# Performance work log

Measured on AMD Instinct MI355X. Metric: run time of the kernel, lower is better.

## Reference

```python
import jax, jax.numpy as jnp
import numpy as np

B, N, K, D, H = 4, 8192, 16, 128, 4
DK = D // H  # key_dim = num_hiddens // num_heads
NEG_INF = -1e9


def setup_inputs() -> dict:
    key = jax.random.key(0)
    ks = jax.random.split(key, 16)
    s = 1.0 / np.sqrt(D)
    return {
        "vertex_feat": jax.random.normal(ks[0], (B, N, D), dtype=jnp.float32),
        "neighbors_idx": jax.random.randint(ks[1], (B, N, K), 0, N, dtype=jnp.int32),
        "valid_lens": jax.random.randint(ks[2], (B, N), 0, K, dtype=jnp.int32),
        # MultiHeadAttention projections (keras EinsumDense with bias)
        "Wq": (jax.random.normal(ks[3], (D, H, DK)) * s).astype(jnp.float32),
        "bq": jnp.zeros((H, DK), jnp.float32),
        "Wk": (jax.random.normal(ks[4], (D, H, DK)) * s).astype(jnp.float32),
        "bk": jnp.zeros((H, DK), jnp.float32),
        "Wv": (jax.random.normal(ks[5], (D, H, DK)) * s).astype(jnp.float32),
        "bv": jnp.zeros((H, DK), jnp.float32),
        "Wo": (jax.random.normal(ks[6], (H, DK, D)) * s).astype(jnp.float32),
        "bo": jnp.zeros((D,), jnp.float32),
        # MLP: Dense(D, relu) -> Dense(D)
        "W1": (jax.random.normal(ks[7], (D, D)) * s).astype(jnp.float32),
        "b1": jnp.zeros((D,), jnp.float32),
        "W2": (jax.random.normal(ks[8], (D, D)) * s).astype(jnp.float32),
        "b2": jnp.zeros((D,), jnp.float32),
    }


def reference(vertex_feat, neighbors_idx, valid_lens,
              Wq, bq, Wk, bk, Wv, bv, Wo, bo, W1, b1, W2, b2):
    # query: [B, N, 1, D]; gathered neighbors (batch_dims=1): [B, N, K, D]
    q = vertex_feat[:, :, None, :]
    neigh = jax.vmap(lambda vf, idx: vf[idx])(vertex_feat, neighbors_idx)
    value = jnp.concatenate([q, neigh], axis=2)  # [B, N, K+1, D]

    # per-head projections
    qh = jnp.einsum('bnqd,dhk->bnqhk', q, Wq) + bq      # [B,N,1,H,DK]
    kh = jnp.einsum('bnsd,dhk->bnshk', value, Wk) + bk  # [B,N,K+1,H,DK]
    vh = jnp.einsum('bnsd,dhk->bnshk', value, Wv) + bv

    # attention over the neighbor axis (attention_axes=(2,))
    scores = jnp.einsum('bnqhk,bnshk->bnhqs', qh, kh) / np.sqrt(DK)  # [B,N,H,1,K+1]
    # mask: positions < valid_lens + 1 (self + valid neighbors)
    pos = jnp.arange(K + 1)[None, None, :]                # [1,1,K+1]
    mask = pos < (valid_lens + 1)[:, :, None]             # [B,N,K+1] bool
    scores = scores + jnp.where(mask, 0.0, NEG_INF)[:, :, None, None, :]
    attn = jax.nn.softmax(scores, axis=-1)                # [B,N,H,1,K+1]

    ctx = jnp.einsum('bnhqs,bnshk->bnqhk', attn, vh)      # [B,N,1,H,DK]
    out = jnp.einsum('bnqhk,hkd->bnqd', ctx, Wo) + bo     # [B,N,1,D]
    out = out[:, :, 0, :]                                  # squeeze -> [B,N,D]

    # MLP (dropout inactive at inference)
    h = jax.nn.relu(out @ W1 + b1)
    new_vertex_feat = h @ W2 + b2
    return new_vertex_feat
```

## Files before the change

kernel.cpp:

```cpp
#include <hip/hip_runtime.h>
#include <math.h>

#define BB 4
#define NN 8192
#define KNB 16
#define DD 128
#define SS 17
#define M_TOT (BB*NN)
#define WPAD 136
#define KVS 256

typedef __attribute__((ext_vector_type(8))) short          bf8;
typedef __attribute__((ext_vector_type(4))) float          f4;
typedef __attribute__((ext_vector_type(4))) unsigned short u16x4;

static __device__ __forceinline__ unsigned short f2bf(float f) {
    unsigned u = __builtin_bit_cast(unsigned, f);
    u += 0x7fffu + ((u >> 16) & 1u);
    return (unsigned short)(u >> 16);
}
static __device__ __forceinline__ float bf2f_s(short h) {
    return __builtin_bit_cast(float, (unsigned)(unsigned short)h << 16);
}

__global__ __launch_bounds__(256) void cvt_wT(
    const float* __restrict__ Wq, const float* __restrict__ Wk,
    const float* __restrict__ Wv, const float* __restrict__ Wo,
    const float* __restrict__ W1, const float* __restrict__ W2,
    unsigned short* __restrict__ out)
{
    int m = blockIdx.x >> 4;
    const float* src = (m == 0) ? Wq : (m == 1) ? Wk : (m == 2) ? Wv
                     : (m == 3) ? Wo : (m == 4) ? W1 : W2;
    unsigned short* dst = out + m * 16384;
    int o = (blockIdx.x & 15) * 1024 + threadIdx.x * 4;
    int n = o >> 7, k = o & 127;
    u16x4 r;
    #pragma unroll
    for (int i = 0; i < 4; ++i) r[i] = f2bf(src[(size_t)(k + i) * 128 + n]);
    *(u16x4*)(dst + o) = r;
}

__global__ __launch_bounds__(256) void qkv_kernel(
    const float* __restrict__ X, const unsigned short* __restrict__ WtT,
    const float* __restrict__ bq, const float* __restrict__ bk,
    const float* __restrict__ bv,
    unsigned short* __restrict__ qh, unsigned short* __restrict__ kv)
{
    __shared__ unsigned short Xs[64 * WPAD];
    __shared__ unsigned short Wb[128 * WPAD];

    const int tid  = threadIdx.x;
    const int row0 = blockIdx.x * 64;

    {
        const f4* Xg = (const f4*)(X + (size_t)row0 * DD);
        #pragma unroll
        for (int i = 0; i < 8; ++i) {
            int idx = tid + i * 256;
            int r = idx >> 5, c4 = idx & 31;
            f4 v = __builtin_nontemporal_load(Xg + idx);
            u16x4 u;
            u[0] = f2bf(v.x); u[1] = f2bf(v.y); u[2] = f2bf(v.z); u[3] = f2bf(v.w);
            *(u16x4*)(Xs + r * WPAD + c4 * 4) = u;
        }
    }
    #pragma unroll
    for (int i = 0; i < 8; ++i) {
        int c = tid + i * 256;
        int n = c >> 4, k8 = c & 15;
        *(bf8*)(Wb + n * WPAD + k8 * 8) = ((const bf8*)WtT)[c];
    }

    const int lane = tid & 63, wv = tid >> 6;
    const int ln = lane & 15, quad = lane >> 4;
    __syncthreads();

    bf8 afr[4];
    #pragma unroll
    for (int s = 0; s < 4; ++s)
        afr[s] = *(const bf8*)(Xs + (wv * 16 + ln) * WPAD + s * 32 + quad * 8);

    #pragma unroll 1
    for (int g = 0; g < 3; ++g) {
        if (g > 0) {
            __syncthreads();
            const bf8* Wn = (const bf8*)(WtT + g * 16384);
            #pragma unroll
            for (int i = 0; i < 8; ++i) {
                int c = tid + i * 256;
                int n = c >> 4, k8 = c & 15;
                *(bf8*)(Wb + n * WPAD + k8 * 8) = Wn[c];
            }
            __syncthreads();
        }

        f4 acc[8] = {};
        #pragma unroll
        for (int t = 0; t < 8; ++t) {
            bf8 bfr[4];
            #pragma unroll
            for (int s = 0; s < 4; ++s)
                bfr[s] = *(const bf8*)(Wb + (t * 16 + ln) * WPAD + s * 32 + quad * 8);
            #pragma unroll
            for (int s = 0; s < 4; ++s)
                acc[t] = __builtin_amdgcn_mfma_f32_16x16x32_bf16(afr[s], bfr[s], acc[t], 0, 0, 0);
        }

        const float* bias = (g == 0) ? bq : (g == 1) ? bk : bv;
        unsigned short* Y;
        int ystride;
        if (g == 0) { Y = qh;       ystride = DD;  }
        else        { Y = kv + (g == 2 ? 128 : 0); ystride = KVS; }

        #pragma unroll
        for (int t = 0; t < 8; ++t) {
            int col = t * 16 + ln;
            float bc = bias[col];
            #pragma unroll
            for (int r = 0; r < 4; ++r) {
                int row = row0 + wv * 16 + quad * 4 + r;
                Y[(size_t)row * ystride + col] = f2bf(acc[t][r] + bc);
            }
        }
    }
}

__global__ __launch_bounds__(256) void attn_kernel(
    const unsigned short* __restrict__ Qh, const unsigned short* __restrict__ KV,
    const int* __restrict__ nbr, const int* __restrict__ vlen,
    unsigned short* __restrict__ Ctx)
{
    const int tid  = threadIdx.x;
    const int vloc = tid >> 4;
    const int ln   = tid & 15;
    const int blk  = blockIdx.x;
    const int b    = (blk & 7) >> 1;
    const int j    = ((blk >> 3) << 1) | (blk & 1);
    const int v    = b * NN + j * 16 + vloc;

    bf8 q8 = __builtin_nontemporal_load((const bf8*)(Qh + (size_t)v * DD + ln * 8));
    float qf[8];
    #pragma unroll
    for (int i = 0; i < 8; ++i) qf[i] = bf2f_s(q8[i]);

    int rows[SS];
    rows[0] = v;
    {
        const int4* np = (const int4*)(nbr + (size_t)v * KNB);
        #pragma unroll
        for (int i = 0; i < 4; ++i) {
            int4 n4 = np[i];
            rows[1 + i * 4 + 0] = b * NN + n4.x;
            rows[1 + i * 4 + 1] = b * NN + n4.y;
            rows[1 + i * 4 + 2] = b * NN + n4.z;
            rows[1 + i * 4 + 3] = b * NN + n4.w;
        }
    }

    const int len = vlen[v];

    float sc[SS];
    #pragma unroll
    for (int s = 0; s < SS; ++s) {
        float p = 0.f;
        if (s <= len) {
            bf8 k8 = *(const bf8*)(KV + (size_t)rows[s] * KVS + ln * 8);
            #pragma unroll
            for (int i = 0; i < 8; ++i) p = fmaf(qf[i], bf2f_s(k8[i]), p);
            p += __shfl_xor(p, 1, 4);
            p += __shfl_xor(p, 2, 4);
        }
        sc[s] = p * 0.17677669529663687f;
    }

    float m = sc[0];
    #pragma unroll
    for (int s = 1; s < SS; ++s) m = (s <= len) ? fmaxf(m, sc[s]) : m;
    float sum = 0.f;
    #pragma unroll
    for (int s = 0; s < SS; ++s) {
        float e = (s <= len) ? __expf(sc[s] - m) : 0.f;
        sc[s] = e;
        sum += e;
    }
    const float inv = 1.f / sum;

    float acc[8] = {};
    #pragma unroll
    for (int s = 0; s < SS; ++s) {
        if (s <= len) {
            bf8 v8 = *(const bf8*)(KV + (size_t)rows[s] * KVS + 128 + ln * 8);
            float w = sc[s] * inv;
            #pragma unroll
            for (int i = 0; i < 8; ++i) acc[i] = fmaf(w, bf2f_s(v8[i]), acc[i]);
        }
    }
    bf8 r;
    #pragma unroll
    for (int i = 0; i < 8; ++i) r[i] = (short)f2bf(acc[i]);
    __builtin_nontemporal_store(r, (bf8*)(Ctx + (size_t)v * DD + ln * 8));
}

__global__ __launch_bounds__(256) void ffn_kernel(
    const unsigned short* __restrict__ Ctxg, const unsigned short* __restrict__ WtT3,
    const float* __restrict__ bo, const float* __restrict__ b1,
    const float* __restrict__ b2, float* __restrict__ Out)
{
    __shared__ unsigned short Ct[64 * WPAD];
    __shared__ unsigned short Wb[128 * WPAD];

    const int tid  = threadIdx.x;
    const int row0 = blockIdx.x * 64;

    {
        const bf8* Cg = (const bf8*)(Ctxg + (size_t)row0 * DD);
        #pragma unroll
        for (int i = 0; i < 4; ++i) {
            int idx = tid + i * 256;
            int r = idx >> 4, c8 = idx & 15;
            *(bf8*)(Ct + r * WPAD + c8 * 8) = __builtin_nontemporal_load(Cg + idx);
        }
    }
    #pragma unroll
    for (int i = 0; i < 8; ++i) {
        int c = tid + i * 256;
        int n = c >> 4, k8 = c & 15;
        *(bf8*)(Wb + n * WPAD + k8 * 8) = ((const bf8*)WtT3)[c];
    }

    const int lane = tid & 63, wv = tid >> 6;
    const int ln = lane & 15, quad = lane >> 4;
    __syncthreads();

    #pragma unroll 1
    for (int g = 0; g < 3; ++g) {
        bf8 afr[4];
        #pragma unroll
        for (int s = 0; s < 4; ++s)
            afr[s] = *(const bf8*)(Ct + (wv * 16 + ln) * WPAD + s * 32 + quad * 8);

        f4 acc[8] = {};
        #pragma unroll
        for (int t = 0; t < 8; ++t) {
            bf8 bfr[4];
            #pragma unroll
            for (int s = 0; s < 4; ++s)
                bfr[s] = *(const bf8*)(Wb + (t * 16 + ln) * WPAD + s * 32 + quad * 8);
            #pragma unroll
            for (int s = 0; s < 4; ++s)
                acc[t] = __builtin_amdgcn_mfma_f32_16x16x32_bf16(afr[s], bfr[s], acc[t], 0, 0, 0);
        }

        __syncthreads();

        const float* bias = (g == 0) ? bo : (g == 1) ? b1 : b2;
        if (g == 2) {
            #pragma unroll
            for (int t = 0; t < 8; ++t) {
                int col = t * 16 + ln;
                float bc = bias[col];
                #pragma unroll
                for (int r = 0; r < 4; ++r) {
                    int row = row0 + wv * 16 + quad * 4 + r;
                    __builtin_nontemporal_store(acc[t][r] + bc,
                                                Out + (size_t)row * DD + col);
                }
            }
        } else {
            const bf8* Wn = (const bf8*)(WtT3 + (g + 1) * 16384);
            #pragma unroll
            for (int i = 0; i < 8; ++i) {
                int c = tid + i * 256;
                int n = c >> 4, k8 = c & 15;
                *(bf8*)(Wb + n * WPAD + k8 * 8) = Wn[c];
            }
            #pragma unroll
            for (int t = 0; t < 8; ++t) {
                int col = t * 16 + ln;
                float bc = bias[col];
                #pragma unroll
                for (int r = 0; r < 4; ++r) {
                    int rloc = wv * 16 + quad * 4 + r;
                    float vv = acc[t][r] + bc;
                    if (g == 1) vv = fmaxf(vv, 0.f);
                    Ct[rloc * WPAD + col] = f2bf(vv);
                }
            }
            __syncthreads();
        }
    }
}

extern "C" void kernel_launch(void* const* d_in, const int* in_sizes, int n_in,
                              void* d_out, int out_size, void* d_ws, size_t ws_size,
                              hipStream_t stream)
{
    const float* vf   = (const float*)d_in[0];
    const int*   nbr  = (const int*)  d_in[1];
    const int*   vlen = (const int*)  d_in[2];
    const float* Wq   = (const float*)d_in[3];
    const float* bq   = (const float*)d_in[4];
    const float* Wk   = (const float*)d_in[5];
    const float* bk   = (const float*)d_in[6];
    const float* Wv   = (const float*)d_in[7];
    const float* bv   = (const float*)d_in[8];
    const float* Wo   = (const float*)d_in[9];
    const float* bo   = (const float*)d_in[10];
    const float* W1   = (const float*)d_in[11];
    const float* b1   = (const float*)d_in[12];
    const float* W2   = (const float*)d_in[13];
    const float* b2   = (const float*)d_in[14];

    float* out = (float*)d_out;

    const size_t SZ = (size_t)M_TOT * DD;
    unsigned short* WtT = (unsigned short*)d_ws;
    unsigned short* qh  = WtT + 6 * 16384;
    unsigned short* kv  = qh + SZ;
    unsigned short* ctx = kv + 2 * SZ;

    cvt_wT<<<96, 256, 0, stream>>>(Wq, Wk, Wv, Wo, W1, W2, WtT);

    qkv_kernel<<<M_TOT / 64, 256, 0, stream>>>(vf, WtT, bq, bk, bv, qh, kv);

    attn_kernel<<<M_TOT / 16, 256, 0, stream>>>(qh, kv, nbr, vlen, ctx);

    ffn_kernel<<<M_TOT / 64, 256, 0, stream>>>(ctx, WtT + 3 * 16384, bo, b1, b2, out);
}
```

Baseline: 142.3 us.

## Batch K/V gathers into registers with branchless masked rows; drop nontemporal hints

The attention kernel now redirects masked neighbor rows to the self row, then issues all 17 K loads up front and all 17 V loads before the softmax, so the gathers overlap instead of being serialized behind per-slot branches. Masked slots still get zero weight, since their scores are excluded from the max and their exponentials are zeroed. Separately, nontemporal loads and stores in the qkv, attention and ffn kernels are replaced with ordinary accesses so the data can stay in cache. The trade-off is higher register pressure from holding 34 bf8 vectors per thread, plus redundant loads for masked slots.

Result: faster. 133.5 us (-6.2%).

```diff
diff --git a/kernel.cpp b/kernel.cpp
--- a/kernel.cpp
+++ b/kernel.cpp
@@ -59,7 +59,7 @@
         for (int i = 0; i < 8; ++i) {
             int idx = tid + i * 256;
             int r = idx >> 5, c4 = idx & 31;
-            f4 v = __builtin_nontemporal_load(Xg + idx);
+            f4 v = Xg[idx];
             u16x4 u;
             u[0] = f2bf(v.x); u[1] = f2bf(v.y); u[2] = f2bf(v.z); u[3] = f2bf(v.w);
             *(u16x4*)(Xs + r * WPAD + c4 * 4) = u;
@@ -139,10 +139,12 @@
     const int j    = ((blk >> 3) << 1) | (blk & 1);
     const int v    = b * NN + j * 16 + vloc;
 
-    bf8 q8 = __builtin_nontemporal_load((const bf8*)(Qh + (size_t)v * DD + ln * 8));
+    bf8 q8 = *(const bf8*)(Qh + (size_t)v * DD + ln * 8);
     float qf[8];
     #pragma unroll
     for (int i = 0; i < 8; ++i) qf[i] = bf2f_s(q8[i]);
+
+    const int len = vlen[v];
 
     int rows[SS];
     rows[0] = v;
@@ -157,22 +159,29 @@
             rows[1 + i * 4 + 3] = b * NN + n4.w;
         }
     }
-
-    const int len = vlen[v];
+    #pragma unroll
+    for (int s = 1; s < SS; ++s) rows[s] = (s <= len) ? rows[s] : rows[0];
+
+    bf8 kreg[SS];
+    #pragma unroll
+    for (int s = 0; s < SS; ++s)
+        kreg[s] = *(const bf8*)(KV + (size_t)rows[s] * KVS + ln * 8);
 
     float sc[SS];
     #pragma unroll
     for (int s = 0; s < SS; ++s) {
         float p = 0.f;
-        if (s <= len) {
-            bf8 k8 = *(const bf8*)(KV + (size_t)rows[s] * KVS + ln * 8);
-            #pragma unroll
-            for (int i = 0; i < 8; ++i) p = fmaf(qf[i], bf2f_s(k8[i]), p);
-            p += __shfl_xor(p, 1, 4);
-            p += __shfl_xor(p, 2, 4);
-        }
+        #pragma unroll
+        for (int i = 0; i < 8; ++i) p = fmaf(qf[i], bf2f_s(kreg[s][i]), p);
+        p += __shfl_xor(p, 1, 4);
+        p += __shfl_xor(p, 2, 4);
         sc[s] = p * 0.17677669529663687f;
     }
+
+    bf8 vreg[SS];
+    #pragma unroll
+    for (int s = 0; s < SS; ++s)
+        vreg[s] = *(const bf8*)(KV + (size_t)rows[s] * KVS + 128 + ln * 8);
 
     float m = sc[0];
     #pragma unroll
@@ -189,17 +198,14 @@
     float acc[8] = {};
     #pragma unroll
     for (int s = 0; s < SS; ++s) {
-        if (s <= len) {
-            bf8 v8 = *(const bf8*)(KV + (size_t)rows[s] * KVS + 128 + ln * 8);
-            float w = sc[s] * inv;
-            #pragma unroll
-            for (int i = 0; i < 8; ++i) acc[i] = fmaf(w, bf2f_s(v8[i]), acc[i]);
-        }
+        float w = sc[s] * inv;
+        #pragma unroll
+        for (int i = 0; i < 8; ++i) acc[i] = fmaf(w, bf2f_s(vreg[s][i]), acc[i]);
     }
     bf8 r;
     #pragma unroll
     for (int i = 0; i < 8; ++i) r[i] = (short)f2bf(acc[i]);
-    __builtin_nontemporal_store(r, (bf8*)(Ctx + (size_t)v * DD + ln * 8));
+    *(bf8*)(Ctx + (size_t)v * DD + ln * 8) = r;
 }
 
 __global__ __launch_bounds__(256) void ffn_kernel(
@@ -219,7 +225,7 @@
         for (int i = 0; i < 4; ++i) {
             int idx = tid + i * 256;
             int r = idx >> 4, c8 = idx & 15;
-            *(bf8*)(Ct + r * WPAD + c8 * 8) = __builtin_nontemporal_load(Cg + idx);
+            *(bf8*)(Ct + r * WPAD + c8 * 8) = Cg[idx];
         }
     }
     #pragma unroll
@@ -263,8 +269,7 @@
                 #pragma unroll
                 for (int r = 0; r < 4; ++r) {
                     int row = row0 + wv * 16 + quad * 4 + r;
-                    __builtin_nontemporal_store(acc[t][r] + bc,
-                                                Out + (size_t)row * DD + col);
+                    Out[(size_t)row * DD + col] = acc[t][r] + bc;
                 }
             }
         } else {
```
